# Kernel optimization log

Measured on AMD Instinct MI355X. Metric: run time of the kernel, lower is better.

The kernel has to match this reference:

```python
import jax, jax.numpy as jnp
import numpy as np

D_MODEL = 2048
HEADDIM = 32
NHEADS = D_MODEL // HEADDIM  # 64
BLOCK = 256
EPS = 1e-4


def segsum(x):
    # x: (..., T) -> (..., T, T) stable segment sums, -inf above diagonal
    T = x.shape[-1]
    xe = jnp.broadcast_to(x[..., None], x.shape + (T,))  # (..., d, e)
    lower = jnp.tril(jnp.ones((T, T), dtype=bool), -1)
    xe = jnp.where(lower, xe, 0.0)
    s = jnp.cumsum(xe, axis=-2)
    incl = jnp.tril(jnp.ones((T, T), dtype=bool), 0)
    return jnp.where(incl, s, -jnp.inf)


def ssd_minimal_discrete(X, A, B, C, block_len):
    # X: (b, L, h, p); A: (b, L, h); B, C: (b, L, h, n). L % block_len == 0.
    b, Lm, h, p = X.shape
    c = Lm // block_len
    Xb = X.reshape(b, c, block_len, h, p)
    Bb = B.reshape(b, c, block_len, h, B.shape[-1])
    Cb = C.reshape(b, c, block_len, h, C.shape[-1])
    Ab = A.reshape(b, c, block_len, h).transpose(0, 3, 1, 2)  # (b, h, c, l)
    A_cumsum = jnp.cumsum(Ab, axis=-1)
    Lmat = jnp.exp(segsum(Ab))  # (b, h, c, l, s)
    # 1. intra-chunk (diagonal block) output
    Y_diag = jnp.einsum('bclhn,bcshn,bhcls,bcshp->bclhp', Cb, Bb, Lmat, Xb)
    # 2. per-chunk states
    decay_states = jnp.exp(A_cumsum[:, :, :, -1:] - A_cumsum)  # (b, h, c, l)
    states = jnp.einsum('bclhn,bhcl,bclhp->bchpn', Bb, decay_states, Xb)
    # 3. inter-chunk recurrence
    init = jnp.zeros_like(states[:, :1])
    states = jnp.concatenate([init, states], axis=1)  # (b, c+1, h, p, n)
    A_last = jnp.pad(A_cumsum[:, :, :, -1], ((0, 0), (0, 0), (1, 0)))  # (b, h, c+1)
    decay_chunk = jnp.exp(segsum(A_last))  # (b, h, c+1, c+1)
    new_states = jnp.einsum('bhzc,bchpn->bzhpn', decay_chunk, states)
    states_in, final_state = new_states[:, :-1], new_states[:, -1]
    # 4. state -> output within chunks
    state_decay_out = jnp.exp(A_cumsum)  # (b, h, c, l)
    Y_off = jnp.einsum('bclhn,bchpn,bhcl->bclhp', Cb, states_in, state_decay_out)
    Y = (Y_diag + Y_off).reshape(b, Lm, h, p)
    return Y, final_state


def setup_inputs() -> dict:
    key = jax.random.key(0)
    k1, k2 = jax.random.split(key)
    Bsz, Lfull, M = 2, 4096, 2048
    hidden_states = jax.random.normal(k1, (Bsz, M, D_MODEL), dtype=jnp.float32)
    # boundaries at even positions: exactly M boundaries per row, position 0 is a boundary
    boundary_mask = jnp.broadcast_to((jnp.arange(Lfull) % 2 == 0)[None, :], (Bsz, Lfull))
    boundary_prob = jax.random.uniform(k2, (Bsz, Lfull, 2), dtype=jnp.float32)
    mask = jnp.ones((Bsz, Lfull), dtype=bool)
    return {"hidden_states": hidden_states, "boundary_mask": boundary_mask,
            "boundary_prob": boundary_prob, "mask": mask}


def reference(hidden_states, boundary_mask, boundary_prob, mask):
    Bsz, Lfull = boundary_mask.shape
    M = hidden_states.shape[1]
    # select boundary-position probabilities, in order, first M
    p = jnp.clip(boundary_prob[..., -1].astype(jnp.float32), EPS, 1.0 - EPS)
    token_idx = jnp.arange(Lfull)[None, :] + (~boundary_mask).astype(jnp.int32) * Lfull
    order = jnp.argsort(token_idx, axis=1, stable=True)
    p_sel = jnp.take_along_axis(p, order[:, :M], axis=1)  # (B, M)
    dt = jnp.log(1.0 / (1.0 - p_sel))
    x = hidden_states.astype(jnp.float32) / dt[..., None]
    Xr = x.reshape(Bsz, M, NHEADS, HEADDIM)
    A_dt = -jnp.broadcast_to(dt[:, :, None], (Bsz, M, NHEADS))  # A = -1, A*dt
    B_ssd = jnp.broadcast_to(p_sel[:, :, None, None], (Bsz, M, NHEADS, 1))
    C_ssd = jnp.ones_like(B_ssd)
    out, _ = ssd_minimal_discrete(Xr, A_dt, B_ssd, C_ssd, BLOCK)
    out = out.reshape(Bsz, M, D_MODEL)
    # plug back: each uncompressed token reads the EMA value of its chunk
    plug = jnp.cumsum(boundary_mask.astype(jnp.int32), axis=1) - 1  # (B, L)
    out = jnp.take_along_axis(out, plug[:, :, None], axis=1)  # (B, L, d_model)
    return out
```

## Files before the change

kernel.cpp:

```cpp
#include <hip/hip_runtime.h>
#include <math.h>

#define BSZ    2
#define LFULL  4096
#define MLEN   2048
#define DMODEL 2048
#define CLIP_EPS 1e-4f
#define CCH    256
#define TCH    8

typedef float f4 __attribute__((ext_vector_type(4)));

__global__ __launch_bounds__(1024, 2) void mega(
    const float* __restrict__ hid, const int* __restrict__ bmask_raw,
    const float* __restrict__ bprob, float* __restrict__ out)
{
  const int tid = threadIdx.x;
  const int j   = tid & 3;
  const int c   = tid >> 2;
  const int bx  = blockIdx.x;
  const int b   = blockIdx.y;

  __shared__ int   s_sel[MLEN];
  __shared__ float s_P[CCH];
  __shared__ f4    s_S[CCH][4];
  __shared__ int   s_wtot[16];
  __shared__ int   s_mode, s_ntrue;

  const int d4 = bx * 4 + j;
  const int o  = b * MLEN + c * TCH;
  const f4* xp = (const f4*)hid + ((size_t)o * DMODEL >> 2) + d4;
  f4 xr[TCH];
  #pragma unroll
  for (int t = 0; t < TCH; ++t) xr[t] = xp[(size_t)t * (DMODEL / 4)];
  #pragma unroll
  for (int t = 0; t < TCH; ++t) asm volatile("" : "+v"(xr[t]));

  if (tid == 0) {
    unsigned w0 = ((const unsigned*)bmask_raw)[0];
    s_mode = (w0 <= 1u) ? 1 : 0;
  }
  __syncthreads();
  const int mode = s_mode;
  const unsigned char* bmask_u8 = (const unsigned char*)bmask_raw;

  const int PER  = LFULL / 1024;
  const int base = tid * PER;

  int cnt = 0;
  {
    #pragma unroll
    for (int i = 0; i < PER; ++i) {
      const int L = base + i;
      const int v = mode ? (bmask_raw[b * LFULL + L] != 0)
                         : (bmask_u8[b * LFULL + L] != 0);
      cnt += v;
    }
  }

  const int lane = tid & 63, wv = tid >> 6;
  int incl = cnt;
  #pragma unroll
  for (int off = 1; off < 64; off <<= 1) {
    const int v = __shfl_up(incl, off, 64);
    if (lane >= off) incl += v;
  }
  if (lane == 63) s_wtot[wv] = incl;
  __syncthreads();
  if (tid == 0) {
    int run = 0;
    #pragma unroll
    for (int w = 0; w < 16; ++w) { const int t = s_wtot[w]; s_wtot[w] = run; run += t; }
    s_ntrue = run;
  }
  __syncthreads();
  const int excl  = (incl - cnt) + s_wtot[wv];
  const int ntrue = s_ntrue;

  {
    int trun = excl;
    #pragma unroll
    for (int i = 0; i < PER; ++i) {
      const int L = base + i;
      const int v = mode ? (bmask_raw[b * LFULL + L] != 0)
                         : (bmask_u8[b * LFULL + L] != 0);
      if (v) {
        if (trun < MLEN) s_sel[trun] = L;
        ++trun;
      } else {
        const int f = L - trun;
        const int slot = ntrue + f;
        if (slot < MLEN) s_sel[slot] = L;
      }
    }
  }
  __syncthreads();

  float w[TCH], e[TCH], cd[TCH];
  {
    float run = 1.0f;
    #pragma unroll
    for (int t = 0; t < TCH; ++t) {
      const int L = s_sel[c * TCH + t];
      float p = bprob[((size_t)b * LFULL + L) * 2 + 1];
      p = fminf(fmaxf(p, CLIP_EPS), 1.0f - CLIP_EPS);
      const float dt = -log1pf(-p);
      w[t] = p / dt;
      e[t] = 1.0f - p;
      run *= e[t];
      cd[t] = run;
    }
  }

  f4 st = {0.f, 0.f, 0.f, 0.f};
  #pragma unroll
  for (int t = 0; t < TCH; ++t) {
    const f4 x = xr[t];
    st.x = fmaf(e[t], st.x, w[t] * x.x);
    st.y = fmaf(e[t], st.y, w[t] * x.y);
    st.z = fmaf(e[t], st.z, w[t] * x.z);
    st.w = fmaf(e[t], st.w, w[t] * x.w);
    xr[t] = st;
  }
  s_S[c][j] = st;
  if (j == 0) s_P[c] = cd[TCH - 1];
  __syncthreads();

  for (int dstep = 1; dstep < CCH; dstep <<= 1) {
    const float pc = s_P[c];
    float pd = 1.0f;
    f4 sd = {0.f, 0.f, 0.f, 0.f};
    if (c >= dstep) { pd = s_P[c - dstep]; sd = s_S[c - dstep][j]; }
    __syncthreads();
    if (c >= dstep) {
      f4 cur = s_S[c][j];
      cur.x = fmaf(pc, sd.x, cur.x);
      cur.y = fmaf(pc, sd.y, cur.y);
      cur.z = fmaf(pc, sd.z, cur.z);
      cur.w = fmaf(pc, sd.w, cur.w);
      s_S[c][j] = cur;
      if (j == 0) s_P[c] = pc * pd;
    }
    __syncthreads();
  }

  f4 H = {0.f, 0.f, 0.f, 0.f};
  if (c > 0) H = s_S[c - 1][j];

  const int nb = (ntrue < MLEN) ? ntrue : MLEN;
  f4* op = (f4*)out + ((size_t)b * LFULL * DMODEL >> 2) + d4;
  #pragma unroll
  for (int t = 0; t < TCH; ++t) {
    const int g = c * TCH + t;
    int ls, le;
    if (nb == 0) {
      ls = (g == 0) ? 0 : LFULL;
      le = (g == 0) ? LFULL : LFULL;
    } else if (g < nb) {
      ls = (g == 0) ? 0 : s_sel[g];
      le = (g == nb - 1) ? LFULL : s_sel[g + 1];
    } else {
      ls = LFULL; le = LFULL;
    }
    f4 y;
    y.x = fmaf(cd[t], H.x, xr[t].x);
    y.y = fmaf(cd[t], H.y, xr[t].y);
    y.z = fmaf(cd[t], H.z, xr[t].z);
    y.w = fmaf(cd[t], H.w, xr[t].w);
    for (int L = ls; L < le; ++L) {
      __builtin_nontemporal_store(y, op + (size_t)L * (DMODEL / 4));
    }
  }
}

extern "C" void kernel_launch(void* const* d_in, const int* in_sizes, int n_in,
                              void* d_out, int out_size, void* d_ws, size_t ws_size,
                              hipStream_t stream) {
  const float* hid   = (const float*)d_in[0];
  const int*   bmask = (const int*)d_in[1];
  const float* bprob = (const float*)d_in[2];
  float*       out   = (float*)d_out;
  (void)d_ws; (void)ws_size;

  mega<<<dim3(DMODEL / 16, BSZ), dim3(1024), 0, stream>>>(hid, bmask, bprob, out);
}
```

Measured before the change: 116.6 us.

## Split fused kernel into scan front-end and separate output-expansion kernel

The single mega kernel is split in two. The first kernel computes the boundary selection, per-chunk weights and the chunk-carry prefix scan, then writes carries and per-token metadata to workspace. The second kernel re-reads the hidden states, recomputes the intra-chunk recurrence and does the scatter of output rows with a much larger grid (2x256x2 blocks of 256 threads). The aim is to spread the dominant output-write phase over many more blocks and free registers in the front kernel. The cost is a second launch, a second read of the hidden input, and the extra carry array G written to and read back from global memory.

```diff
diff --git a/kernel.cpp b/kernel.cpp
--- a/kernel.cpp
+++ b/kernel.cpp
@@ -11,9 +11,12 @@
 
 typedef float f4 __attribute__((ext_vector_type(4)));
 
-__global__ __launch_bounds__(1024, 2) void mega(
+__global__ __launch_bounds__(1024, 4) void mega_front(
     const float* __restrict__ hid, const int* __restrict__ bmask_raw,
-    const float* __restrict__ bprob, float* __restrict__ out)
+    const float* __restrict__ bprob,
+    int* __restrict__ Ls, int* __restrict__ Le,
+    float* __restrict__ wA, float* __restrict__ eA,
+    float* __restrict__ cde, float* __restrict__ G)
 {
   const int tid = threadIdx.x;
   const int j   = tid & 3;
@@ -48,14 +51,12 @@
   const int base = tid * PER;
 
   int cnt = 0;
-  {
-    #pragma unroll
-    for (int i = 0; i < PER; ++i) {
-      const int L = base + i;
-      const int v = mode ? (bmask_raw[b * LFULL + L] != 0)
-                         : (bmask_u8[b * LFULL + L] != 0);
-      cnt += v;
-    }
+  #pragma unroll
+  for (int i = 0; i < PER; ++i) {
+    const int L = base + i;
+    const int v = mode ? (bmask_raw[b * LFULL + L] != 0)
+                       : (bmask_u8[b * LFULL + L] != 0);
+    cnt += v;
   }
 
   const int lane = tid & 63, wv = tid >> 6;
@@ -120,7 +121,6 @@
     st.y = fmaf(e[t], st.y, w[t] * x.y);
     st.z = fmaf(e[t], st.z, w[t] * x.z);
     st.w = fmaf(e[t], st.w, w[t] * x.w);
-    xr[t] = st;
   }
   s_S[c][j] = st;
   if (j == 0) s_P[c] = cd[TCH - 1];
@@ -147,26 +147,73 @@
   f4 H = {0.f, 0.f, 0.f, 0.f};
   if (c > 0) H = s_S[c - 1][j];
 
-  const int nb = (ntrue < MLEN) ? ntrue : MLEN;
-  f4* op = (f4*)out + ((size_t)b * LFULL * DMODEL >> 2) + d4;
+  ((f4*)G)[((size_t)(b * CCH + c) * DMODEL >> 2) + d4] = H;
+
+  if (bx == 0 && j == 0) {
+    const int nb = (ntrue < MLEN) ? ntrue : MLEN;
+    #pragma unroll
+    for (int t = 0; t < TCH; ++t) {
+      const int g = c * TCH + t;
+      wA[b * MLEN + g]  = w[t];
+      eA[b * MLEN + g]  = e[t];
+      cde[b * MLEN + g] = cd[t];
+      int ls, le;
+      if (nb == 0) {
+        ls = (g == 0) ? 0 : LFULL;
+        le = (g == 0) ? LFULL : LFULL;
+      } else if (g < nb) {
+        ls = (g == 0) ? 0 : s_sel[g];
+        le = (g == nb - 1) ? LFULL : s_sel[g + 1];
+      } else {
+        ls = LFULL; le = LFULL;
+      }
+      Ls[b * MLEN + g] = ls;
+      Le[b * MLEN + g] = le;
+    }
+  }
+}
+
+__global__ __launch_bounds__(256) void k3_out(
+    const float* __restrict__ hid, const float* __restrict__ wA,
+    const float* __restrict__ eA, const float* __restrict__ cde,
+    const float* __restrict__ G,
+    const int* __restrict__ Ls, const int* __restrict__ Le,
+    float* __restrict__ out)
+{
+  const int tid = threadIdx.x;
+  const int c = blockIdx.y;
+  const int b = blockIdx.z;
+
+  __shared__ float s_w[TCH], s_e[TCH], s_c[TCH];
+  __shared__ int   s_ls[TCH], s_le[TCH];
+  const int o = b * MLEN + c * TCH;
+  if (tid < TCH)          { s_w[tid] = wA[o + tid];  s_ls[tid] = Ls[o + tid]; }
+  else if (tid < 2 * TCH) { const int t = tid - TCH;     s_e[t] = eA[o + t]; s_le[t] = Le[o + t]; }
+  else if (tid < 3 * TCH) { const int t = tid - 2 * TCH; s_c[t] = cde[o + t]; }
+  __syncthreads();
+
+  const int d4 = blockIdx.x * 256 + tid;
+
+  const f4 H = ((const f4*)G)[((size_t)(b * CCH + c) * DMODEL >> 2) + d4];
+
+  const f4* xp = (const f4*)hid + ((size_t)(b * MLEN + c * TCH) * DMODEL >> 2) + d4;
+  f4*       op = (f4*)out + ((size_t)b * LFULL * DMODEL >> 2) + d4;
+
+  f4 st = {0.f, 0.f, 0.f, 0.f};
   #pragma unroll
   for (int t = 0; t < TCH; ++t) {
-    const int g = c * TCH + t;
-    int ls, le;
-    if (nb == 0) {
-      ls = (g == 0) ? 0 : LFULL;
-      le = (g == 0) ? LFULL : LFULL;
-    } else if (g < nb) {
-      ls = (g == 0) ? 0 : s_sel[g];
-      le = (g == nb - 1) ? LFULL : s_sel[g + 1];
-    } else {
-      ls = LFULL; le = LFULL;
-    }
+    const f4 x = xp[(size_t)t * (DMODEL / 4)];
+    const float w = s_w[t], e = s_e[t], cd = s_c[t];
+    st.x = fmaf(e, st.x, w * x.x);
+    st.y = fmaf(e, st.y, w * x.y);
+    st.z = fmaf(e, st.z, w * x.z);
+    st.w = fmaf(e, st.w, w * x.w);
     f4 y;
-    y.x = fmaf(cd[t], H.x, xr[t].x);
-    y.y = fmaf(cd[t], H.y, xr[t].y);
-    y.z = fmaf(cd[t], H.z, xr[t].z);
-    y.w = fmaf(cd[t], H.w, xr[t].w);
+    y.x = fmaf(cd, H.x, st.x);
+    y.y = fmaf(cd, H.y, st.y);
+    y.z = fmaf(cd, H.z, st.z);
+    y.w = fmaf(cd, H.w, st.w);
+    const int ls = s_ls[t], le = s_le[t];
     for (int L = ls; L < le; ++L) {
       __builtin_nontemporal_store(y, op + (size_t)L * (DMODEL / 4));
     }
@@ -180,7 +227,20 @@
   const int*   bmask = (const int*)d_in[1];
   const float* bprob = (const float*)d_in[2];
   float*       out   = (float*)d_out;
-  (void)d_ws; (void)ws_size;
-
-  mega<<<dim3(DMODEL / 16, BSZ), dim3(1024), 0, stream>>>(hid, bmask, bprob, out);
+
+  char* ws = (char*)d_ws;
+  const size_t SZI = (size_t)BSZ * MLEN * sizeof(int);
+  const size_t SZF = (size_t)BSZ * MLEN * sizeof(float);
+  int*   Ls  = (int*)(ws);
+  int*   Le  = (int*)(ws + SZI);
+  float* wA  = (float*)(ws + 2 * SZI);
+  float* eA  = (float*)(ws + 2 * SZI + SZF);
+  float* cde = (float*)(ws + 2 * SZI + 2 * SZF);
+  float* G   = (float*)(ws + 2 * SZI + 3 * SZF + 4096);
+
+  mega_front<<<dim3(DMODEL / 16, BSZ), dim3(1024), 0, stream>>>(
+      hid, bmask, bprob, Ls, Le, wA, eA, cde, G);
+
+  k3_out<<<dim3(2, CCH, BSZ), dim3(256), 0, stream>>>(
+      hid, wA, eA, cde, G, Ls, Le, out);
 }
```

After: 121.7 us. +4.4%, slower.
